# Performance work log

Hardware: AMD Instinct MI355X
Metric: run time of the kernel (lower is better)

Reference implementation:

```python
import jax, jax.numpy as jnp
import numpy as np

B, L, V = 1024, 50, 26
E1, E2, CD, H, D = 21, 42, 60, 100, 200
EMB_D = E1 + E2  # 63


def _maxpool1d(x, k=5, pad=1):
    # torch MaxPool1d(kernel_size=k, stride=1, padding=pad): pads with -inf
    return jax.lax.reduce_window(x, -jnp.inf, jax.lax.max,
                                 (1, 1, k), (1, 1, 1),
                                 ((0, 0), (0, 0), (pad, pad)))


def _conv_block(x0, w, b):
    # x0: (B, C_in, L); w: (CD, C_in, h) -> conv1d VALID + ReLU + maxpool + right-pad to L=50
    y = jax.lax.conv_general_dilated(x0, w, (1,), 'VALID',
                                     dimension_numbers=('NCH', 'OIH', 'NCH'))
    y = jax.nn.relu(y + b[None, :, None])
    y = _maxpool1d(y)
    return jnp.pad(y, ((0, 0), (0, 0), (0, L - y.shape[2])))


def _lstm_dir(xs, wih, whh, bih, bhh):
    # xs: (B, T, In); torch gate order i, f, g, o
    gx = xs @ wih.T + (bih + bhh)  # (B, T, 4H)
    bs = xs.shape[0]
    h0 = jnp.zeros((bs, H), xs.dtype)

    def step(carry, g_t):
        h, c = carry
        g = g_t + h @ whh.T
        i, f, gg, o = jnp.split(g, 4, axis=-1)
        c = jax.nn.sigmoid(f) * c + jax.nn.sigmoid(i) * jnp.tanh(gg)
        h = jax.nn.sigmoid(o) * jnp.tanh(c)
        return (h, c), h

    _, hs = jax.lax.scan(step, (h0, h0), jnp.swapaxes(gx, 0, 1))
    return jnp.swapaxes(hs, 0, 1)  # (B, T, H)


def _forward(x, emb1, emb2, cw2, cb2, cw3, cb3, cw8, cb8,
             wih_f, whh_f, bih_f, bhh_f, wih_b, whh_b, bih_b, bhh_b,
             wq, bq, wk, bk, wv, bv, pos_bias, dw1, db1, dw2, db2):
    # embeddings -> (B, EMB_D, L)
    x0 = jnp.concatenate([jnp.transpose(emb1[x], (0, 2, 1)),
                          jnp.transpose(emb2[x], (0, 2, 1))], axis=1)
    # three conv branches, padded to L and concatenated on channels
    x1 = jnp.concatenate([_conv_block(x0, cw2, cb2),
                          _conv_block(x0, cw3, cb3),
                          _conv_block(x0, cw8, cb8)], axis=1)  # (B, 3*CD, L)
    # dropout is identity at inference
    merge = jnp.concatenate([x0, x1], axis=1)  # (B, 243, L)
    seq = jnp.transpose(merge, (0, 2, 1))      # (B, L, 243)
    # bidirectional LSTM -> (B, L, 200)
    h_f = _lstm_dir(seq, wih_f, whh_f, bih_f, bhh_f)
    h_b = _lstm_dir(seq[:, ::-1], wih_b, whh_b, bih_b, bhh_b)[:, ::-1]
    h = jnp.concatenate([h_f, h_b], axis=-1)
    # AFT-full attention. exp(k + pb) factorizes as exp(k) * exp(pb);
    # num[b,i,d] = sum_j exp(pb[i,j]) * exp(k[b,j,d]) * v[b,j,d]
    q = h @ wq.T + bq
    k = h @ wk.T + bk
    v = h @ wv.T + bv
    ek = jnp.exp(k)                 # (B, n, D)
    wpb = jnp.exp(pos_bias)         # (n, n)
    num = jnp.einsum('ij,bjd->bid', wpb, ek * v)
    den = jnp.einsum('ij,bjd->bid', wpb, ek)
    att = jax.nn.sigmoid(q) * (num / den)  # (B, n, D)
    # dense head
    flat = att.reshape(att.shape[0], -1)   # (B, 10000)
    hid = jax.nn.relu(flat @ dw1.T + db1)
    return jax.nn.sigmoid(hid @ dw2.T + db2)  # (B, output_length)


def setup_inputs():
    key = jax.random.key(0)
    ks = jax.random.split(key, 30)
    f = lambda i, shape, s=0.02: jax.random.normal(ks[i], shape, jnp.float32) * s
    return {
        'x': jax.random.randint(ks[0], (B, L), 0, V),
        'emb1': f(1, (V, E1), 1.0),
        'emb2': f(2, (V, E2), 1.0),
        'cw2': f(3, (CD, EMB_D, 2)), 'cb2': f(4, (CD,)),
        'cw3': f(5, (CD, EMB_D, 3)), 'cb3': f(6, (CD,)),
        'cw8': f(7, (CD, EMB_D, 8)), 'cb8': f(8, (CD,)),
        'wih_f': f(9, (4 * H, 243)), 'whh_f': f(10, (4 * H, H)),
        'bih_f': f(11, (4 * H,)), 'bhh_f': f(12, (4 * H,)),
        'wih_b': f(13, (4 * H, 243)), 'whh_b': f(14, (4 * H, H)),
        'bih_b': f(15, (4 * H,)), 'bhh_b': f(16, (4 * H,)),
        'wq': f(17, (D, D)), 'bq': jnp.zeros((D,), jnp.float32),
        'wk': f(18, (D, D)), 'bk': jnp.zeros((D,), jnp.float32),
        'wv': f(19, (D, D)), 'bv': jnp.zeros((D,), jnp.float32),
        'pos_bias': jnp.ones((L, L), jnp.float32) + f(20, (L, L), 0.1),
        'dw1': f(21, (128, L * D)), 'db1': f(22, (128,)),
        'dw2': f(23, (5, 128)), 'db2': f(24, (5,)),
    }


def reference(x, emb1, emb2, cw2, cb2, cw3, cb3, cw8, cb8,
              wih_f, whh_f, bih_f, bhh_f, wih_b, whh_b, bih_b, bhh_b,
              wq, bq, wk, bk, wv, bv, pos_bias, dw1, db1, dw2, db2):
    return _forward(x, emb1, emb2, cw2, cb2, cw3, cb3, cw8, cb8,
                    wih_f, whh_f, bih_f, bhh_f, wih_b, whh_b, bih_b, bhh_b,
                    wq, bq, wk, bk, wv, bv, pos_bias, dw1, db1, dw2, db2)
```

## Files before the change

### kernel.cpp

```cpp
#include <hip/hip_runtime.h>
#include <cstdint>
#include <cstddef>

#define B_    1024
#define L_    50
#define EMB_  63
#define CD_   60
#define H_    100
#define G4_   400
#define DH_   200
#define NHID_ 128
#define KD_   10000
#define KDP_  10240
#define NSPL_ 16

typedef __attribute__((ext_vector_type(8))) short short8;
typedef __attribute__((ext_vector_type(4))) float f32x4;

__device__ __forceinline__ float sigf(float x){ return 1.f/(1.f+expf(-x)); }
__device__ __forceinline__ unsigned short f2bf(float f){
  unsigned int x = __float_as_uint(f);
  unsigned int r = x + 0x7fffu + ((x>>16)&1u);
  return (unsigned short)(r>>16);
}
__device__ __forceinline__ float bf2f(unsigned short u){
  return __uint_as_float(((unsigned int)u)<<16);
}
__device__ __forceinline__ void load_lds16(const void* g, void* l){
  __builtin_amdgcn_global_load_lds((const __attribute__((address_space(1))) void*)g,
                                   (__attribute__((address_space(3))) void*)l, 16, 0, 0);
}

__global__ __launch_bounds__(256) void k_pack(
    const float* __restrict__ wih_f, const float* __restrict__ bih_f, const float* __restrict__ bhh_f,
    const float* __restrict__ wih_b, const float* __restrict__ bih_b, const float* __restrict__ bhh_b,
    const float* __restrict__ whh_f, const float* __restrict__ whh_b,
    const float* __restrict__ wq, const float* __restrict__ bq,
    const float* __restrict__ wk, const float* __restrict__ bk,
    const float* __restrict__ wv, const float* __restrict__ bv,
    const float* __restrict__ dw1,
    unsigned short* __restrict__ wihp, float* __restrict__ bihp,
    unsigned short* __restrict__ wqkvp, float* __restrict__ bqkvp,
    unsigned short* __restrict__ whhpk, unsigned short* __restrict__ dw1p)
{
  int i = blockIdx.x*256 + threadIdx.x;
  if (i < 204800) {
    int d = i / 102400, rem = i % 102400, r = rem >> 8, k = rem & 255;
    const float* src = d ? wih_b : wih_f;
    wihp[i] = f2bf((k < 243) ? src[r*243 + k] : 0.f);
  } else if ((i -= 204800) < 800) {
    bihp[i] = (i < 400) ? (bih_f[i] + bhh_f[i]) : (bih_b[i-400] + bhh_b[i-400]);
  } else if ((i -= 800) < 150528) {
    int s = i / 50176, rem = i % 50176, n = rem / 224, k = rem % 224;
    const float* w = (s==0) ? wq : (s==1) ? wk : wv;
    wqkvp[i] = f2bf((n < 200 && k < 200) ? w[n*200 + k] : 0.f);
  } else if ((i -= 150528) < 672) {
    int s = i / 224, n = i % 224;
    const float* bb = (s==0) ? bq : (s==1) ? bk : bv;
    bqkvp[i] = (n < 200) ? bb[n] : 0.f;
  } else if ((i -= 672) < 114688) {
    int d = i / 57344, rem = i % 57344, n = rem >> 7, k = rem & 127;
    const float* src = d ? whh_b : whh_f;
    whhpk[i] = f2bf((n < 400 && k < 100) ? src[n*100 + k] : 0.f);
  } else if ((i -= 114688) < 1310720) {
    int n = i / KDP_, k = i % KDP_;
    dw1p[i] = f2bf((k < KD_) ? dw1[(size_t)n*KD_ + k] : 0.f);
  }
}

template<int KH>
__device__ __forceinline__ void conv_branch(
    const float (&x0s)[EMB_][64], float (&ys)[49][65],
    const float* __restrict__ w, const float* __restrict__ cb,
    unsigned short* __restrict__ seq, int b, int co, int tid)
{
  const int Lc = 51 - KH;
  const int Lp = Lc - 2;
  const int nt8 = (Lc + 7) >> 3;
  const int ntask = 30 * nt8;
  for (int task = tid; task < ntask; task += 256) {
    int o2 = task / nt8, tc = (task % nt8) << 3;
    const int o0 = o2*2;
    float acc[2][8];
    {
      float b0v = cb[o0], b1v = cb[o0+1];
      #pragma unroll
      for (int j = 0; j < 8; ++j) { acc[0][j] = b0v; acc[1][j] = b1v; }
    }
    for (int c = 0; c < EMB_; ++c) {
      float xw[16];
      const float* xr = &x0s[c][tc];
      *(float4*)&xw[0]  = *(const float4*)&xr[0];
      *(float4*)&xw[4]  = *(const float4*)&xr[4];
      *(float4*)&xw[8]  = *(const float4*)&xr[8];
      *(float4*)&xw[12] = *(const float4*)&xr[12];
      const float* wr0 = &w[(size_t)(o0*EMB_ + c)*KH];
      const float* wr1 = &w[(size_t)((o0+1)*EMB_ + c)*KH];
      #pragma unroll
      for (int tau = 0; tau < KH; ++tau) {
        float w0 = wr0[tau], w1 = wr1[tau];
        #pragma unroll
        for (int j = 0; j < 8; ++j) {
          acc[0][j] = fmaf(xw[tau+j], w0, acc[0][j]);
          acc[1][j] = fmaf(xw[tau+j], w1, acc[1][j]);
        }
      }
    }
    #pragma unroll
    for (int j = 0; j < 8; ++j) {
      int t = tc + j;
      if (t < Lc) {
        ys[t][o0]   = fmaxf(acc[0][j], 0.f);
        ys[t][o0+1] = fmaxf(acc[1][j], 0.f);
      }
    }
  }
  __syncthreads();
  for (int idx = tid; idx < L_*CD_; idx += 256) {
    int l = idx / CD_, o = idx - (idx/CD_)*CD_;
    float vm = 0.f;
    if (l < Lp) {
      int lo = (l-1 < 0) ? 0 : l-1;
      int hi = (l+3 >= Lc) ? Lc-1 : l+3;
      for (int t = lo; t <= hi; ++t) vm = fmaxf(vm, ys[t][o]);
    }
    seq[((size_t)b*L_ + l)*256 + co + o] = f2bf(vm);
  }
  __syncthreads();
}

__global__ __launch_bounds__(256) void k_embconv(
    const int* __restrict__ x, const float* __restrict__ emb1, const float* __restrict__ emb2,
    const float* __restrict__ cw2, const float* __restrict__ cb2,
    const float* __restrict__ cw3, const float* __restrict__ cb3,
    const float* __restrict__ cw8, const float* __restrict__ cb8,
    unsigned short* __restrict__ seq)
{
  __shared__ float x0s[EMB_][64];
  __shared__ float ys[49][65];
  __shared__ int   xs[L_];
  const int b = blockIdx.x, tid = threadIdx.x;
  if (tid < L_) xs[tid] = x[b*L_ + tid];
  __syncthreads();
  for (int idx = tid; idx < EMB_*64; idx += 256) {
    int c = idx >> 6, l = idx & 63;
    float v = 0.f;
    if (l < L_) { int e = xs[l]; v = (c < 21) ? emb1[e*21 + c] : emb2[e*42 + (c-21)]; }
    x0s[c][l] = v;
  }
  __syncthreads();
  for (int idx = tid; idx < L_*EMB_; idx += 256) {
    int l = idx / EMB_, c = idx - (idx/EMB_)*EMB_;
    seq[((size_t)b*L_ + l)*256 + c] = f2bf(x0s[c][l]);
  }
  for (int idx = tid; idx < L_*13; idx += 256) {
    int l = idx / 13, p = idx - (idx/13)*13;
    seq[((size_t)b*L_ + l)*256 + 243 + p] = 0;
  }
  __syncthreads();
  conv_branch<2>(x0s, ys, cw2, cb2, seq, b, EMB_,          tid);
  conv_branch<3>(x0s, ys, cw3, cb3, seq, b, EMB_ + CD_,    tid);
  conv_branch<8>(x0s, ys, cw8, cb8, seq, b, EMB_ + 2*CD_,  tid);
}

template<int NF, int KSTEPS, int ACT, int OUTMODE>
__global__ __launch_bounds__(256) void k_gemm_mfma(
    const unsigned short* __restrict__ A,
    const unsigned short* __restrict__ W,
    const float* __restrict__ bias,
    void* __restrict__ C, int Nstride, int Nreal)
{
  constexpr int BN = NF*16;
  constexpr int KA = KSTEPS*32;
  constexpr int TU = 512 + BN*4;
  __shared__ __attribute__((aligned(16))) unsigned short As[512*8];
  __shared__ __attribute__((aligned(16))) unsigned short Ws[BN*32];
  const int tid = threadIdx.x;
  const int lane = tid & 63, w = tid >> 6;
  const int m0 = blockIdx.x*128, n0 = blockIdx.y*BN;
  const int c = lane >> 4, r16 = lane & 15;
  f32x4 acc[2][NF];
  #pragma unroll
  for (int i = 0; i < 2; ++i)
    #pragma unroll
    for (int j = 0; j < NF; ++j) acc[i][j] = (f32x4){0.f,0.f,0.f,0.f};

  for (int ks = 0; ks < KSTEPS; ++ks) {
    const int k0 = ks*32;
    #pragma unroll
    for (int it = 0; it*256 < TU; ++it) {
      const int u0 = it*256 + w*64;
      if (u0 < TU) {
        if (u0 < 512) {
          const int u = u0 + lane;
          const int cc = u >> 7, row = u & 127;
          load_lds16(&A[(size_t)(m0+row)*KA + k0 + cc*8], (char*)As + (size_t)u0*16);
        } else {
          const int v2 = u0 - 512 + lane;
          const int n = v2 >> 2, cc = v2 & 3;
          load_lds16(&W[(size_t)(n0+n)*KA + k0 + cc*8], (char*)Ws + (size_t)(u0-512)*16);
        }
      }
    }
    __syncthreads();
    short8 a0 = *(const short8*)&As[(c*128 + w*32 + r16)*8];
    short8 a1 = *(const short8*)&As[(c*128 + w*32 + 16 + r16)*8];
    #pragma unroll
    for (int nf = 0; nf < NF; ++nf) {
      short8 bfr = *(const short8*)&Ws[((nf*16 + r16)*4 + c)*8];
      acc[0][nf] = __builtin_amdgcn_mfma_f32_16x16x32_bf16(a0, bfr, acc[0][nf], 0, 0, 0);
      acc[1][nf] = __builtin_amdgcn_mfma_f32_16x16x32_bf16(a1, bfr, acc[1][nf], 0, 0, 0);
    }
    __syncthreads();
  }
  const int rg = lane >> 4;
  #pragma unroll
  for (int mf = 0; mf < 2; ++mf) {
    #pragma unroll
    for (int nf = 0; nf < NF; ++nf) {
      const int colp = n0 + nf*16 + r16;
      const float bs = bias[colp];
      #pragma unroll
      for (int r = 0; r < 4; ++r) {
        const int row = m0 + w*32 + mf*16 + rg*4 + r;
        float val = acc[mf][nf][r] + bs;
        if (ACT == 1) val = sigf(val);
        else if (ACT == 2) val = expf(val);
        if (OUTMODE == 0) {
          if (colp < Nreal) ((float*)C)[(size_t)row*Nstride + colp] = val;
        } else {
          ((unsigned short*)C)[(size_t)row*Nstride + colp] = f2bf(val);
        }
      }
    }
  }
}

__global__ __launch_bounds__(256) void k_scan(
    const unsigned short* __restrict__ gx,
    const unsigned short* __restrict__ whhpk,
    unsigned short* __restrict__ hout)
{
  __shared__ __attribute__((aligned(16))) unsigned short h_s[16][136];
  __shared__ float g_s[8][448];
  const int dir = blockIdx.y;
  const int b0 = blockIdx.x * 8;
  const int tid = threadIdx.x;
  const int lane = tid & 63, w = tid >> 6;
  const int r16 = lane & 15, c = lane >> 4;

  short8 bfr[7][4];
  {
    const unsigned short* wb = whhpk + (size_t)dir*448*128;
    #pragma unroll
    for (int nf = 0; nf < 7; ++nf)
      #pragma unroll
      for (int ks = 0; ks < 4; ++ks)
        bfr[nf][ks] = *(const short8*)&wb[(size_t)(w*112 + nf*16 + r16)*128 + ks*32 + c*8];
  }
  for (int idx = tid; idx < 16*136; idx += 256) ((unsigned short*)h_s)[idx] = 0;
  float cst[4] = {0.f,0.f,0.f,0.f};
  const int kh = tid % 100;
  const int r0 = tid / 100;
  const bool pbact = (tid < 200);
  __syncthreads();

  for (int t = 0; t < L_; ++t) {
    const int tp = dir ? (L_-1-t) : t;
    f32x4 acc[7];
    #pragma unroll
    for (int nf = 0; nf < 7; ++nf) acc[nf] = (f32x4){0.f,0.f,0.f,0.f};
    short8 afr[4];
    #pragma unroll
    for (int ks = 0; ks < 4; ++ks)
      afr[ks] = *(const short8*)&h_s[r16][ks*32 + c*8];
    #pragma unroll
    for (int ks = 0; ks < 4; ++ks)
      #pragma unroll
      for (int nf = 0; nf < 7; ++nf)
        acc[nf] = __builtin_amdgcn_mfma_f32_16x16x32_bf16(afr[ks], bfr[nf][ks], acc[nf], 0, 0, 0);
    unsigned short gxr[4][4];
    if (pbact) {
      #pragma unroll
      for (int i = 0; i < 4; ++i) {
        const int row = r0 + 2*i;
        const size_t gbase = ((size_t)(b0+row)*L_ + tp)*800 + (size_t)dir*400 + kh;
        #pragma unroll
        for (int g = 0; g < 4; ++g) gxr[i][g] = gx[gbase + 100*g];
      }
    }
    if (c < 2) {
      #pragma unroll
      for (int nf = 0; nf < 7; ++nf) {
        const int col = w*112 + nf*16 + r16;
        #pragma unroll
        for (int r = 0; r < 4; ++r)
          g_s[c*4 + r][col] = acc[nf][r];
      }
    }
    __syncthreads();
    if (pbact) {
      #pragma unroll
      for (int i = 0; i < 4; ++i) {
        const int row = r0 + 2*i;
        float gi = g_s[row][kh]       + bf2f(gxr[i][0]);
        float gf = g_s[row][kh + 100] + bf2f(gxr[i][1]);
        float gg = g_s[row][kh + 200] + bf2f(gxr[i][2]);
        float go = g_s[row][kh + 300] + bf2f(gxr[i][3]);
        float cn = sigf(gf)*cst[i] + sigf(gi)*tanhf(gg);
        cst[i] = cn;
        float hn = sigf(go)*tanhf(cn);
        unsigned short hb16 = f2bf(hn);
        h_s[row][kh] = hb16;
        hout[((size_t)(b0+row)*L_ + tp)*224 + dir*H_ + kh] = hb16;
      }
    }
    if (dir == 0 && tid < 192) {
      int r = tid / 24, p = tid - (tid/24)*24;
      hout[((size_t)(b0+r)*L_ + tp)*224 + 200 + p] = 0;
    }
    __syncthreads();
  }
}

__global__ __launch_bounds__(256) void k_attn(
    const float* __restrict__ sq, const float* __restrict__ ek, const float* __restrict__ v,
    const float* __restrict__ pos_bias, unsigned short* __restrict__ att)
{
  extern __shared__ char smem[];
  unsigned short* eks = (unsigned short*)smem;
  unsigned short* evs = eks + L_*DH_;
  float* wpT = (float*)(smem + 40000);
  const int b = blockIdx.x, tid = threadIdx.x;
  const size_t base = (size_t)b*KD_;
  const size_t obase = (size_t)b*KDP_;
  for (int idx = tid; idx < L_*DH_; idx += 256) {
    float e = ek[base + idx];
    eks[idx] = f2bf(e);
    evs[idx] = f2bf(e * v[base + idx]);
  }
  for (int idx = tid; idx < 50*56; idx += 256) {
    int j = idx / 56, i = idx - (idx/56)*56;
    wpT[idx] = (i < L_) ? expf(pos_bias[i*L_ + j]) : 0.f;
  }
  __syncthreads();
  if (tid < 175) {
    const int ioct = tid / 25, doct = tid - (tid/25)*25;
    const int i0 = ioct*8, d0 = doct*8;
    float num[8][8], den[8][8];
    #pragma unroll
    for (int i = 0; i < 8; ++i)
      #pragma unroll
      for (int j = 0; j < 8; ++j) { num[i][j] = 0.f; den[i][j] = 0.f; }
    for (int j = 0; j < L_; ++j) {
      float wv8[8], ee8[8], ev8[8];
      *(float4*)&wv8[0] = *(const float4*)&wpT[j*56 + i0];
      *(float4*)&wv8[4] = *(const float4*)&wpT[j*56 + i0 + 4];
      short8 ee = *(const short8*)&eks[j*DH_ + d0];
      short8 ev = *(const short8*)&evs[j*DH_ + d0];
      #pragma unroll
      for (int u = 0; u < 8; ++u) {
        ee8[u] = bf2f((unsigned short)ee[u]);
        ev8[u] = bf2f((unsigned short)ev[u]);
      }
      #pragma unroll
      for (int ii = 0; ii < 8; ++ii)
        #pragma unroll
        for (int dd = 0; dd < 8; ++dd) {
          num[ii][dd] = fmaf(wv8[ii], ev8[dd], num[ii][dd]);
          den[ii][dd] = fmaf(wv8[ii], ee8[dd], den[ii][dd]);
        }
    }
    for (int ii = 0; ii < 8; ++ii) {
      int i = i0 + ii;
      if (i >= L_) break;
      #pragma unroll
      for (int d4 = 0; d4 < 2; ++d4) {
        int d = d0 + d4*4;
        float4 s4 = *(const float4*)&sq[base + (size_t)i*DH_ + d];
        att[obase + (size_t)i*DH_ + d + 0] = f2bf(s4.x * num[ii][d4*4+0] / den[ii][d4*4+0]);
        att[obase + (size_t)i*DH_ + d + 1] = f2bf(s4.y * num[ii][d4*4+1] / den[ii][d4*4+1]);
        att[obase + (size_t)i*DH_ + d + 2] = f2bf(s4.z * num[ii][d4*4+2] / den[ii][d4*4+2]);
        att[obase + (size_t)i*DH_ + d + 3] = f2bf(s4.w * num[ii][d4*4+3] / den[ii][d4*4+3]);
      }
    }
  }
  for (int idx = tid; idx < KDP_ - KD_; idx += 256) att[obase + KD_ + idx] = 0;
}

__global__ __launch_bounds__(256) void k_dense1m(
    const unsigned short* __restrict__ att,
    const unsigned short* __restrict__ dw1p,
    float* __restrict__ part)
{
  __shared__ __attribute__((aligned(16))) unsigned short As[512*8];
  __shared__ __attribute__((aligned(16))) unsigned short Ws[128*32];
  const int tid = threadIdx.x;
  const int lane = tid & 63, w = tid >> 6;
  const int m0 = blockIdx.x*128;
  const int koff = blockIdx.y*640;
  const int c = lane >> 4, r16 = lane & 15;
  f32x4 acc[2][8];
  #pragma unroll
  for (int i = 0; i < 2; ++i)
    #pragma unroll
    for (int j = 0; j < 8; ++j) acc[i][j] = (f32x4){0.f,0.f,0.f,0.f};

  for (int ks = 0; ks < 20; ++ks) {
    const int k0 = koff + ks*32;
    #pragma unroll
    for (int it = 0; it < 4; ++it) {
      const int u0 = it*256 + w*64;
      if (u0 < 512) {
        const int u = u0 + lane;
        const int cc = u >> 7, row = u & 127;
        load_lds16(&att[(size_t)(m0+row)*KDP_ + k0 + cc*8], (char*)As + (size_t)u0*16);
      } else {
        const int v2 = u0 - 512 + lane;
        const int n = v2 >> 2, cc = v2 & 3;
        load_lds16(&dw1p[(size_t)n*KDP_ + k0 + cc*8], (char*)Ws + (size_t)(u0-512)*16);
      }
    }
    __syncthreads();
    short8 a0 = *(const short8*)&As[(c*128 + w*32 + r16)*8];
    short8 a1 = *(const short8*)&As[(c*128 + w*32 + 16 + r16)*8];
    #pragma unroll
    for (int nf = 0; nf < 8; ++nf) {
      short8 bfr = *(const short8*)&Ws[((nf*16 + r16)*4 + c)*8];
      acc[0][nf] = __builtin_amdgcn_mfma_f32_16x16x32_bf16(a0, bfr, acc[0][nf], 0, 0, 0);
      acc[1][nf] = __builtin_amdgcn_mfma_f32_16x16x32_bf16(a1, bfr, acc[1][nf], 0, 0, 0);
    }
    __syncthreads();
  }
  const int rg = lane >> 4;
  #pragma unroll
  for (int mf = 0; mf < 2; ++mf)
    #pragma unroll
    for (int nf = 0; nf < 8; ++nf) {
      const int col = nf*16 + r16;
      #pragma unroll
      for (int r = 0; r < 4; ++r) {
        const int row = m0 + w*32 + mf*16 + rg*4 + r;
        part[((size_t)blockIdx.y*B_ + row)*NHID_ + col] = acc[mf][nf][r];
      }
    }
}

__global__ __launch_bounds__(128) void k_dense2(
    const float* __restrict__ part, const float* __restrict__ db1,
    const float* __restrict__ dw2, const float* __restrict__ db2,
    float* __restrict__ out)
{
  __shared__ float hid[NHID_];
  const int b = blockIdx.x, o = threadIdx.x;
  float s = db1[o];
  #pragma unroll
  for (int sl = 0; sl < NSPL_; ++sl) s += part[((size_t)sl*B_ + b)*NHID_ + o];
  hid[o] = fmaxf(s, 0.f);
  __syncthreads();
  if (o < 5) {
    float acc = db2[o];
    for (int j = 0; j < NHID_; ++j) acc = fmaf(hid[j], dw2[o*NHID_ + j], acc);
    out[b*5 + o] = sigf(acc);
  }
}

extern "C" void kernel_launch(void* const* d_in, const int* in_sizes, int n_in,
                              void* d_out, int out_size, void* d_ws, size_t ws_size,
                              hipStream_t stream)
{
  const int*   x     = (const int*)  d_in[0];
  const float* emb1  = (const float*)d_in[1];
  const float* emb2  = (const float*)d_in[2];
  const float* cw2   = (const float*)d_in[3];
  const float* cb2   = (const float*)d_in[4];
  const float* cw3   = (const float*)d_in[5];
  const float* cb3   = (const float*)d_in[6];
  const float* cw8   = (const float*)d_in[7];
  const float* cb8   = (const float*)d_in[8];
  const float* wih_f = (const float*)d_in[9];
  const float* whh_f = (const float*)d_in[10];
  const float* bih_f = (const float*)d_in[11];
  const float* bhh_f = (const float*)d_in[12];
  const float* wih_b = (const float*)d_in[13];
  const float* whh_b = (const float*)d_in[14];
  const float* bih_b = (const float*)d_in[15];
  const float* bhh_b = (const float*)d_in[16];
  const float* wq    = (const float*)d_in[17];
  const float* bq    = (const float*)d_in[18];
  const float* wk    = (const float*)d_in[19];
  const float* bk    = (const float*)d_in[20];
  const float* wv    = (const float*)d_in[21];
  const float* bv    = (const float*)d_in[22];
  const float* pos_bias = (const float*)d_in[23];
  const float* dw1   = (const float*)d_in[24];
  const float* db1   = (const float*)d_in[25];
  const float* dw2   = (const float*)d_in[26];
  const float* db2   = (const float*)d_in[27];
  (void)in_sizes; (void)n_in; (void)out_size;

  char* base = (char*)d_ws;
  size_t off = 0;
  auto alloc = [&](size_t bytes) -> char* {
    char* p = base + off;
    off = (off + bytes + 255) & ~(size_t)255;
    return p;
  };
  unsigned short* seqb  = (unsigned short*)alloc(51200UL*256*2);
  unsigned short* gxb   = (unsigned short*)alloc(51200UL*800*2);
  unsigned short* hb    = (unsigned short*)alloc(51200UL*224*2);
  float*          sqb   = (float*)alloc(51200UL*200*4);
  float*          ekb   = (float*)alloc(51200UL*200*4);
  float*          vb    = (float*)alloc(51200UL*200*4);
  unsigned short* wihp  = (unsigned short*)alloc(204800UL*2);
  float*          bihp  = (float*)alloc(800UL*4);
  unsigned short* wqkvp = (unsigned short*)alloc(150528UL*2);
  float*          bqkvp = (float*)alloc(672UL*4);
  unsigned short* whhpk = (unsigned short*)alloc(114688UL*2);
  unsigned short* dw1p  = (unsigned short*)alloc(1310720UL*2);
  if (off > ws_size) return;
  unsigned short* attb = (unsigned short*)gxb;
  float* part = (float*)seqb;

  hipFuncSetAttribute(reinterpret_cast<const void*>(k_attn),
                      hipFuncAttributeMaxDynamicSharedMemorySize, 51200);

  k_pack<<<dim3(6962), 256, 0, stream>>>(wih_f, bih_f, bhh_f, wih_b, bih_b, bhh_b,
                                         whh_f, whh_b, wq, bq, wk, bk, wv, bv, dw1,
                                         wihp, bihp, wqkvp, bqkvp, whhpk, dw1p);
  k_embconv<<<dim3(1024), 256, 0, stream>>>(x, emb1, emb2, cw2, cb2, cw3, cb3, cw8, cb8, seqb);
  k_gemm_mfma<5, 8, 0, 1><<<dim3(400, 10), 256, 0, stream>>>(seqb, wihp, bihp, gxb, 800, 800);
  k_scan<<<dim3(128, 2), 256, 0, stream>>>(gxb, whhpk, hb);
  k_gemm_mfma<7, 7, 1, 0><<<dim3(400, 2), 256, 0, stream>>>(hb, wqkvp,          bqkvp,       sqb, 200, 200);
  k_gemm_mfma<7, 7, 2, 0><<<dim3(400, 2), 256, 0, stream>>>(hb, wqkvp + 50176,  bqkvp + 224, ekb, 200, 200);
  k_gemm_mfma<7, 7, 0, 0><<<dim3(400, 2), 256, 0, stream>>>(hb, wqkvp + 100352, bqkvp + 448, vb,  200, 200);
  k_attn<<<dim3(1024), 256, 51200, stream>>>(sqb, ekb, vb, pos_bias, attb);
  k_dense1m<<<dim3(8, NSPL_), 256, 0, stream>>>(attb, dw1p, part);
  k_dense2<<<dim3(1024), 128, 0, stream>>>(part, db1, dw2, db2, (float*)d_out);
}
```

Before: 546.7 us.

## Rewrite conv branches as bf16 MFMA implicit GEMM over packed weights

Replaces the scalar FMA per-branch convolution with one implicit-GEMM kernel that handles two batch rows per block and computes all three conv branches together using bf16 MFMA. Conv weights are packed once into a tau-major bf16 layout, and k-steps beyond each branch's kernel width are skipped. Post-ReLU values are stored as bf16 and max-pooled by integer comparison, which is valid because all values are non-negative. This trades fp32 accumulation inputs for bf16 precision on the conv operands and uses much more LDS per block.

```diff
diff --git a/kernel.cpp b/kernel.cpp
--- a/kernel.cpp
+++ b/kernel.cpp
@@ -39,9 +39,13 @@
     const float* __restrict__ wk, const float* __restrict__ bk,
     const float* __restrict__ wv, const float* __restrict__ bv,
     const float* __restrict__ dw1,
+    const float* __restrict__ cw2, const float* __restrict__ cb2,
+    const float* __restrict__ cw3, const float* __restrict__ cb3,
+    const float* __restrict__ cw8, const float* __restrict__ cb8,
     unsigned short* __restrict__ wihp, float* __restrict__ bihp,
     unsigned short* __restrict__ wqkvp, float* __restrict__ bqkvp,
-    unsigned short* __restrict__ whhpk, unsigned short* __restrict__ dw1p)
+    unsigned short* __restrict__ whhpk, unsigned short* __restrict__ dw1p,
+    unsigned short* __restrict__ cwp, float* __restrict__ cwb)
 {
   int i = blockIdx.x*256 + threadIdx.x;
   if (i < 204800) {
@@ -65,102 +69,120 @@
   } else if ((i -= 114688) < 1310720) {
     int n = i / KDP_, k = i % KDP_;
     dw1p[i] = f2bf((k < KD_) ? dw1[(size_t)n*KD_ + k] : 0.f);
-  }
-}
-
-template<int KH>
-__device__ __forceinline__ void conv_branch(
-    const float (&x0s)[EMB_][64], float (&ys)[49][65],
-    const float* __restrict__ w, const float* __restrict__ cb,
-    unsigned short* __restrict__ seq, int b, int co, int tid)
-{
-  const int Lc = 51 - KH;
-  const int Lp = Lc - 2;
-  const int nt8 = (Lc + 7) >> 3;
-  const int ntask = 30 * nt8;
-  for (int task = tid; task < ntask; task += 256) {
-    int o2 = task / nt8, tc = (task % nt8) << 3;
-    const int o0 = o2*2;
-    float acc[2][8];
-    {
-      float b0v = cb[o0], b1v = cb[o0+1];
-      #pragma unroll
-      for (int j = 0; j < 8; ++j) { acc[0][j] = b0v; acc[1][j] = b1v; }
-    }
-    for (int c = 0; c < EMB_; ++c) {
-      float xw[16];
-      const float* xr = &x0s[c][tc];
-      *(float4*)&xw[0]  = *(const float4*)&xr[0];
-      *(float4*)&xw[4]  = *(const float4*)&xr[4];
-      *(float4*)&xw[8]  = *(const float4*)&xr[8];
-      *(float4*)&xw[12] = *(const float4*)&xr[12];
-      const float* wr0 = &w[(size_t)(o0*EMB_ + c)*KH];
-      const float* wr1 = &w[(size_t)((o0+1)*EMB_ + c)*KH];
-      #pragma unroll
-      for (int tau = 0; tau < KH; ++tau) {
-        float w0 = wr0[tau], w1 = wr1[tau];
-        #pragma unroll
-        for (int j = 0; j < 8; ++j) {
-          acc[0][j] = fmaf(xw[tau+j], w0, acc[0][j]);
-          acc[1][j] = fmaf(xw[tau+j], w1, acc[1][j]);
+  } else if ((i -= 1310720) < 98304) {
+    int n = i >> 9, k = i & 511;
+    int tau = k >> 6, c = k & 63;
+    float v = 0.f;
+    if (c < 63) {
+      if (n < 60)       { if (tau < 2) v = cw2[(n*63 + c)*2 + tau]; }
+      else if (n < 120) { if (tau < 3) v = cw3[((n-60)*63 + c)*3 + tau]; }
+      else if (n < 180) { if (tau < 8) v = cw8[((n-120)*63 + c)*8 + tau]; }
+    }
+    cwp[i] = f2bf(v);
+  } else if ((i -= 98304) < 192) {
+    cwb[i] = (i < 60) ? cb2[i] : (i < 120) ? cb3[i-60] : (i < 180) ? cb8[i-120] : 0.f;
+  }
+}
+
+__global__ __launch_bounds__(256) void k_embconv2(
+    const int* __restrict__ x, const float* __restrict__ emb1, const float* __restrict__ emb2,
+    const unsigned short* __restrict__ cwp, const float* __restrict__ cwb,
+    unsigned short* __restrict__ seq)
+{
+  extern __shared__ char smem[];
+  unsigned short (*x0T)[72][72]  = (unsigned short(*)[72][72])smem;
+  unsigned short (*Wst)[192][8]  = (unsigned short(*)[192][8])(smem + 20736);
+  unsigned short (*ys)[50][192]  = (unsigned short(*)[50][192])(smem + 33024);
+  const int tid = threadIdx.x;
+  const int lane = tid & 63, w = tid >> 6;
+  const int r16 = lane & 15, c4 = lane >> 4;
+  const int b0 = blockIdx.x * 2;
+
+  for (int idx = tid; idx < 2*72*72; idx += 256) {
+    int lb = idx / 5184, rem = idx % 5184, t = rem / 72, c = rem % 72;
+    float v = 0.f;
+    if (t < L_ && c < EMB_) {
+      int e = x[(b0+lb)*L_ + t];
+      v = (c < 21) ? emb1[e*21 + c] : emb2[e*42 + (c-21)];
+    }
+    x0T[lb][t][c] = f2bf(v);
+  }
+  __syncthreads();
+
+  for (int idx = tid; idx < 2*L_*EMB_; idx += 256) {
+    int lb = idx / (L_*EMB_), rem = idx % (L_*EMB_), l = rem / EMB_, c = rem % EMB_;
+    seq[((size_t)(b0+lb)*L_ + l)*256 + c] = x0T[lb][l][c];
+  }
+  for (int idx = tid; idx < 2*L_*13; idx += 256) {
+    int lb = idx / (L_*13), rem = idx % (L_*13), l = rem / 13, p = rem % 13;
+    seq[((size_t)(b0+lb)*L_ + l)*256 + 243 + p] = 0;
+  }
+
+  f32x4 acc[2][12];
+  #pragma unroll
+  for (int i = 0; i < 2; ++i)
+    #pragma unroll
+    for (int j = 0; j < 12; ++j) acc[i][j] = (f32x4){0.f,0.f,0.f,0.f};
+
+  for (int ks = 0; ks < 16; ++ks) {
+    const int k0 = ks*32;
+    const int tau = ks >> 1, c0 = (ks & 1)*32;
+    #pragma unroll
+    for (int it = 0; it < 3; ++it) {
+      const int u0 = it*256 + w*64;
+      const int u = u0 + lane;
+      const int cc = u / 192, n = u % 192;
+      load_lds16(&cwp[(size_t)n*512 + k0 + cc*8], (char*)Wst + (size_t)u0*16);
+    }
+    __syncthreads();
+    #pragma unroll
+    for (int mf = 0; mf < 2; ++mf) {
+      const int row = w*32 + mf*16 + r16;
+      const int lb = row >> 6, t = row & 63;
+      short8 a = *(const short8*)&x0T[lb][t + tau][c0 + c4*8];
+      #pragma unroll
+      for (int nf = 0; nf < 12; ++nf) {
+        if (nf < 3 ? (ks < 4) : (nf < 7 ? (ks < 6) : true)) {
+          short8 bfr = *(const short8*)&Wst[c4][nf*16 + r16][0];
+          acc[mf][nf] = __builtin_amdgcn_mfma_f32_16x16x32_bf16(a, bfr, acc[mf][nf], 0, 0, 0);
         }
       }
     }
-    #pragma unroll
-    for (int j = 0; j < 8; ++j) {
-      int t = tc + j;
-      if (t < Lc) {
-        ys[t][o0]   = fmaxf(acc[0][j], 0.f);
-        ys[t][o0+1] = fmaxf(acc[1][j], 0.f);
+    __syncthreads();
+  }
+
+  const int rg = lane >> 4;
+  #pragma unroll
+  for (int mf = 0; mf < 2; ++mf) {
+    #pragma unroll
+    for (int nf = 0; nf < 12; ++nf) {
+      const int col = nf*16 + r16;
+      const float bs = cwb[col];
+      #pragma unroll
+      for (int r = 0; r < 4; ++r) {
+        const int row = w*32 + mf*16 + rg*4 + r;
+        const int lb = row >> 6, t = row & 63;
+        if (t < L_) ys[lb][t][col] = f2bf(fmaxf(acc[mf][nf][r] + bs, 0.f));
       }
     }
   }
   __syncthreads();
-  for (int idx = tid; idx < L_*CD_; idx += 256) {
-    int l = idx / CD_, o = idx - (idx/CD_)*CD_;
-    float vm = 0.f;
-    if (l < Lp) {
+
+  for (int idx = tid; idx < 2*L_*180; idx += 256) {
+    int lb = idx / 9000, rem = idx % 9000, l = rem / 180, n = rem % 180;
+    int br = n / 60;
+    int Lc = (br == 0) ? 49 : (br == 1) ? 48 : 43;
+    unsigned short vm = 0;
+    if (l < Lc - 2) {
       int lo = (l-1 < 0) ? 0 : l-1;
-      int hi = (l+3 >= Lc) ? Lc-1 : l+3;
-      for (int t = lo; t <= hi; ++t) vm = fmaxf(vm, ys[t][o]);
-    }
-    seq[((size_t)b*L_ + l)*256 + co + o] = f2bf(vm);
-  }
-  __syncthreads();
-}
-
-__global__ __launch_bounds__(256) void k_embconv(
-    const int* __restrict__ x, const float* __restrict__ emb1, const float* __restrict__ emb2,
-    const float* __restrict__ cw2, const float* __restrict__ cb2,
-    const float* __restrict__ cw3, const float* __restrict__ cb3,
-    const float* __restrict__ cw8, const float* __restrict__ cb8,
-    unsigned short* __restrict__ seq)
-{
-  __shared__ float x0s[EMB_][64];
-  __shared__ float ys[49][65];
-  __shared__ int   xs[L_];
-  const int b = blockIdx.x, tid = threadIdx.x;
-  if (tid < L_) xs[tid] = x[b*L_ + tid];
-  __syncthreads();
-  for (int idx = tid; idx < EMB_*64; idx += 256) {
-    int c = idx >> 6, l = idx & 63;
-    float v = 0.f;
-    if (l < L_) { int e = xs[l]; v = (c < 21) ? emb1[e*21 + c] : emb2[e*42 + (c-21)]; }
-    x0s[c][l] = v;
-  }
-  __syncthreads();
-  for (int idx = tid; idx < L_*EMB_; idx += 256) {
-    int l = idx / EMB_, c = idx - (idx/EMB_)*EMB_;
-    seq[((size_t)b*L_ + l)*256 + c] = f2bf(x0s[c][l]);
-  }
-  for (int idx = tid; idx < L_*13; idx += 256) {
-    int l = idx / 13, p = idx - (idx/13)*13;
-    seq[((size_t)b*L_ + l)*256 + 243 + p] = 0;
-  }
-  __syncthreads();
-  conv_branch<2>(x0s, ys, cw2, cb2, seq, b, EMB_,          tid);
-  conv_branch<3>(x0s, ys, cw3, cb3, seq, b, EMB_ + CD_,    tid);
-  conv_branch<8>(x0s, ys, cw8, cb8, seq, b, EMB_ + 2*CD_,  tid);
+      int hi = (l+3 > Lc-1) ? Lc-1 : l+3;
+      for (int t = lo; t <= hi; ++t) {
+        unsigned short u = ys[lb][t][n];
+        vm = (u > vm) ? u : vm;
+      }
+    }
+    seq[((size_t)(b0+lb)*L_ + l)*256 + EMB_ + n] = vm;
+  }
 }
 
 template<int NF, int KSTEPS, int ACT, int OUTMODE>
@@ -518,17 +540,22 @@
   float*          bqkvp = (float*)alloc(672UL*4);
   unsigned short* whhpk = (unsigned short*)alloc(114688UL*2);
   unsigned short* dw1p  = (unsigned short*)alloc(1310720UL*2);
+  unsigned short* cwp   = (unsigned short*)alloc(98304UL*2);
+  float*          cwb   = (float*)alloc(192UL*4);
   if (off > ws_size) return;
   unsigned short* attb = (unsigned short*)gxb;
   float* part = (float*)seqb;
 
   hipFuncSetAttribute(reinterpret_cast<const void*>(k_attn),
                       hipFuncAttributeMaxDynamicSharedMemorySize, 51200);
-
-  k_pack<<<dim3(6962), 256, 0, stream>>>(wih_f, bih_f, bhh_f, wih_b, bih_b, bhh_b,
+  hipFuncSetAttribute(reinterpret_cast<const void*>(k_embconv2),
+                      hipFuncAttributeMaxDynamicSharedMemorySize, 71424);
+
+  k_pack<<<dim3(7347), 256, 0, stream>>>(wih_f, bih_f, bhh_f, wih_b, bih_b, bhh_b,
                                          whh_f, whh_b, wq, bq, wk, bk, wv, bv, dw1,
-                                         wihp, bihp, wqkvp, bqkvp, whhpk, dw1p);
-  k_embconv<<<dim3(1024), 256, 0, stream>>>(x, emb1, emb2, cw2, cb2, cw3, cb3, cw8, cb8, seqb);
+                                         cw2, cb2, cw3, cb3, cw8, cb8,
+                                         wihp, bihp, wqkvp, bqkvp, whhpk, dw1p, cwp, cwb);
+  k_embconv2<<<dim3(512), 256, 71424, stream>>>(x, emb1, emb2, cwp, cwb, seqb);
   k_gemm_mfma<5, 8, 0, 1><<<dim3(400, 10), 256, 0, stream>>>(seqb, wihp, bihp, gxb, 800, 800);
   k_scan<<<dim3(128, 2), 256, 0, stream>>>(gxb, whhpk, hb);
   k_gemm_mfma<7, 7, 1, 0><<<dim3(400, 2), 256, 0, stream>>>(hb, wqkvp,          bqkvp,       sqb, 200, 200);
```

After: 486.7 us. -11.0%, faster.
